# Optimization experiments

Measured on AMD Instinct MI355X. Metric: run time of the kernel, lower is better.

## Reference

```python
import jax, jax.numpy as jnp
import numpy as np

E = 128          # embedding_dim
H = 128          # decoder_hidden_dim
N = 200000       # number of candidate nodes


def setup_inputs() -> dict:
    key = jax.random.key(0)
    k0, k1, k2, k3, k4, k5 = jax.random.split(key, 6)
    return {
        "current_node_emb": jax.random.normal(k0, (1, E), jnp.float32),
        "context_emb": jax.random.normal(k1, (1, E), jnp.float32),
        "candidate_node_embs": jax.random.normal(k2, (N, E), jnp.float32),
        "Wq": jax.random.normal(k3, (H, 2 * E), jnp.float32) * 0.05,  # nn.Linear(2E->H, bias=False) weight
        "Wk": jax.random.normal(k4, (H, E), jnp.float32) * 0.05,      # nn.Linear(E->H, bias=False) weight
        "mask": jax.random.randint(k5, (1, N), 0, 2, jnp.int32),
    }


def reference(current_node_emb, context_emb, candidate_node_embs, Wq, Wk, mask):
    # combined_input = cat([current, context], dim=1) -> [1, 2E]
    combined = jnp.concatenate([current_node_emb, context_emb], axis=1)
    query = combined @ Wq.T                      # [1, H]
    keys = candidate_node_embs @ Wk.T            # [N, H]
    attn_scores = query @ keys.T                 # [1, N]
    masked = jnp.where(mask == 0, -jnp.inf, attn_scores)
    probs = jax.nn.softmax(masked, axis=1)       # [1, N]

    n = probs.shape[1]
    k = min(50, max(1, int(0.5 * n)))            # static Python int -> jit-friendly
    top_probs, _ = jax.lax.top_k(probs, k)       # [1, k]
    threshold = top_probs[:, -1:]                # [1, 1]
    top_mask = probs >= threshold
    filtered = probs * top_mask
    filtered = filtered / (jnp.sum(filtered, axis=1, keepdims=True) + 1e-10)

    log_probs_all = jnp.log(filtered + 1e-10)    # [1, N]
    # Categorical(filtered): true-zero probability outside top-k
    logits = jnp.where(filtered > 0, jnp.log(filtered), -jnp.inf)
    action_idx = jax.random.categorical(jax.random.key(42), logits, axis=1)  # [1]
    log_prob_action = jnp.take_along_axis(logits, action_idx[:, None], axis=1)[:, 0]  # [1]
    return (log_probs_all, log_prob_action, action_idx)
```

## Files before the change

### kernel.cpp

```cpp
#include <hip/hip_runtime.h>
#include <math.h>


#define CAP 4096
#define NEG_INF (-__builtin_inff())

__device__ __forceinline__ unsigned int f2ord(float f){
  unsigned int b = __float_as_uint(f);
  return (b & 0x80000000u) ? ~b : (b | 0x80000000u);
}
__device__ __forceinline__ unsigned int rotl32(unsigned int x, int d){
  return (x << d) | (x >> (32 - d));
}

__device__ float gumbel_from_idx(unsigned int idx){
  unsigned int x0 = 0u, x1 = idx;
  const unsigned int ks0 = 0u, ks1 = 42u;
  const unsigned int ks2 = 0u ^ 42u ^ 0x1BD11BDAu;
  x0 += ks0; x1 += ks1;
#define TF_RND(r) { x0 += x1; x1 = rotl32(x1, (r)); x1 ^= x0; }
  TF_RND(13) TF_RND(15) TF_RND(26) TF_RND(6)
  x0 += ks1; x1 += ks2 + 1u;
  TF_RND(17) TF_RND(29) TF_RND(16) TF_RND(24)
  x0 += ks2; x1 += ks0 + 2u;
  TF_RND(13) TF_RND(15) TF_RND(26) TF_RND(6)
  x0 += ks0; x1 += ks1 + 3u;
  TF_RND(17) TF_RND(29) TF_RND(16) TF_RND(24)
  x0 += ks1; x1 += ks2 + 4u;
  TF_RND(13) TF_RND(15) TF_RND(26) TF_RND(6)
  x0 += ks2; x1 += ks0 + 5u;
#undef TF_RND
  unsigned int bits = x0 ^ x1;
  unsigned int fb = (bits >> 9) | 0x3f800000u;
  float f = __uint_as_float(fb) - 1.0f;
  float u = (f < 1.17549435e-38f) ? 1.17549435e-38f : f;
  return -logf(-logf(u));
}

__global__ void k_prep(const float* __restrict__ cur, const float* __restrict__ ctx,
                       const float* __restrict__ Wq, const float* __restrict__ Wk,
                       float* __restrict__ v, unsigned int* __restrict__ hist,
                       unsigned int* __restrict__ scal_u){
  __shared__ float comb[256];
  __shared__ float q[128];
  int t = threadIdx.x;
  for (int k = t; k < 2048; k += 256) hist[k] = 0u;
  if (t < 8) scal_u[t] = 0u;
  comb[t] = (t < 128) ? cur[t] : ctx[t - 128];
  __syncthreads();
  if (t < 128){
    float acc = 0.f;
    const float* row = Wq + t * 256;
    for (int j = 0; j < 256; ++j) acc = fmaf(row[j], comb[j], acc);
    q[t] = acc;
  }
  __syncthreads();
  if (t < 128){
    float acc = 0.f;
    for (int h = 0; h < 128; ++h) acc = fmaf(q[h], Wk[h * 128 + t], acc);
    v[t] = acc;
  }
}

__global__ __launch_bounds__(256) void k_score(const float* __restrict__ cand,
    const int* __restrict__ mask, const float* __restrict__ v,
    float* __restrict__ scores, int N){
  int t = threadIdx.x;
  int lane = t & 63, wave = t >> 6;
  int hi = lane >> 5, hl = lane & 31;
  float4 v4 = ((const float4*)v)[hl];
  const float4* cp = (const float4*)cand;
  int base = (blockIdx.x * 4 + wave) * 16;
  float p[8];
  #pragma unroll
  for (int k = 0; k < 8; ++k){
    int r = base + 2 * k + hi;
    r = (r < N) ? r : (N - 1);
    float4 c = cp[(size_t)r * 32 + hl];
    p[k] = fmaf(c.x, v4.x, fmaf(c.y, v4.y, fmaf(c.z, v4.z, c.w * v4.w)));
  }
  #pragma unroll
  for (int k = 0; k < 8; ++k){
    p[k] += __shfl_xor(p[k], 1, 64);
    p[k] += __shfl_xor(p[k], 2, 64);
    p[k] += __shfl_xor(p[k], 4, 64);
    p[k] += __shfl_xor(p[k], 8, 64);
    p[k] += __shfl_xor(p[k], 16, 64);
  }
  float sv = p[0];
  #pragma unroll
  for (int k = 1; k < 8; ++k) sv = (hl == k) ? p[k] : sv;
  if (hl < 8){
    int r = base + 2 * hl + hi;
    if (r < N) scores[r] = mask[r] ? sv : NEG_INF;
  }
}

__global__ __launch_bounds__(256) void k_hist(const float* __restrict__ scores,
    unsigned int* __restrict__ hist, unsigned int* __restrict__ scal_u,
    int N, int ktop){
  __shared__ unsigned int lhist[2048];
  __shared__ float wsum[4];
  __shared__ int is_last;
  int t = threadIdx.x;
  int lane = t & 63, wave = t >> 6;
  for (int k = t; k < 2048; k += 256) lhist[k] = 0u;
  __syncthreads();
  float ez = 0.f;
  int i0 = (blockIdx.x * 256 + t) * 4;
  if (i0 + 3 < N){
    float4 s4 = *(const float4*)(scores + i0);
    float ss[4] = {s4.x, s4.y, s4.z, s4.w};
    #pragma unroll
    for (int e = 0; e < 4; ++e){
      if (ss[e] > NEG_INF){
        atomicAdd(&lhist[f2ord(ss[e]) >> 21], 1u);
        ez += expf(ss[e]);
      }
    }
  } else {
    for (int e = 0; e < 4; ++e){
      int i = i0 + e;
      if (i < N){
        float s = scores[i];
        if (s > NEG_INF){ atomicAdd(&lhist[f2ord(s) >> 21], 1u); ez += expf(s); }
      }
    }
  }
  #pragma unroll
  for (int off = 32; off; off >>= 1) ez += __shfl_xor(ez, off, 64);
  if (lane == 0) wsum[wave] = ez;
  __syncthreads();
  for (int k = t; k < 2048; k += 256){
    unsigned int c = lhist[k];
    if (c) atomicAdd(&hist[k], c);
  }
  if (t == 0) atomicAdd((float*)scal_u + 3, wsum[0] + wsum[1] + wsum[2] + wsum[3]);
  __syncthreads();
  if (t == 0){
    __threadfence();
    unsigned int old = atomicAdd(&scal_u[6], 1u);
    is_last = (old == gridDim.x - 1u);
  }
  __syncthreads();
  if (!is_last) return;
  __threadfence();
  __shared__ unsigned int suf[256];
  __shared__ int csel_sh;
  unsigned int csum = 0;
  for (int k = 0; k < 8; ++k) csum += hist[t * 8 + k];
  suf[t] = csum;
  if (t == 0) csel_sh = -1;
  __syncthreads();
  for (int d = 1; d < 256; d <<= 1){
    unsigned int add = (t + d < 256) ? suf[t + d] : 0u;
    __syncthreads();
    suf[t] += add;
    __syncthreads();
  }
  unsigned int st = suf[t];
  unsigned int sn = (t < 255) ? suf[t + 1] : 0u;
  if (st >= (unsigned)ktop && sn < (unsigned)ktop) csel_sh = t;
  __syncthreads();
  if (t == 0){
    int b_sel = 0;
    if (csel_sh >= 0){
      int c = csel_sh;
      unsigned int cum = (c < 255) ? suf[c + 1] : 0u;
      for (int b = 8 * c + 7; b >= 8 * c; --b){
        cum += hist[b];
        if (cum >= (unsigned)ktop){ b_sel = b; break; }
      }
    }
    scal_u[1] = ((unsigned int)b_sel) << 21;
  }
}

__global__ __launch_bounds__(256) void k_gather(const float* __restrict__ scores,
    unsigned int* __restrict__ scal_u, unsigned int* __restrict__ buf_idx,
    float* __restrict__ buf_s, float* __restrict__ out, int N, int ktop){
  int t = threadIdx.x;
  unsigned int u_lo = scal_u[1];
  int i0 = (blockIdx.x * 256 + t) * 4;
  if (i0 + 3 < N){
    float4 s4 = *(const float4*)(scores + i0);
    float ss[4] = {s4.x, s4.y, s4.z, s4.w};
    #pragma unroll
    for (int e = 0; e < 4; ++e){
      float s = ss[e];
      if (s > NEG_INF && f2ord(s) >= u_lo){
        unsigned int pos = atomicAdd(&scal_u[0], 1u);
        if (pos < CAP){ buf_idx[pos] = (unsigned int)(i0 + e); buf_s[pos] = s; }
      }
    }
  } else {
    for (int e = 0; e < 4; ++e){
      int i = i0 + e;
      if (i < N){
        float s = scores[i];
        if (s > NEG_INF && f2ord(s) >= u_lo){
          unsigned int pos = atomicAdd(&scal_u[0], 1u);
          if (pos < CAP){ buf_idx[pos] = (unsigned int)i; buf_s[pos] = s; }
        }
      }
    }
  }
  __syncthreads();
  __shared__ int is_last;
  if (t == 0){
    __threadfence();
    unsigned int old = atomicAdd(&scal_u[7], 1u);
    is_last = (old == gridDim.x - 1u);
  }
  __syncthreads();
  if (!is_last) return;
  __threadfence();
  float* scal_f = (float*)scal_u;
  __shared__ float s_lds[CAP];
  __shared__ float thr_sh;
  __shared__ float wred[4];
  __shared__ float rv[4], rl[4];
  __shared__ unsigned int ri[4];
  int C = (int)scal_u[0]; if (C > CAP) C = CAP;
  for (int j = t; j < C; j += 256) s_lds[j] = buf_s[j];
  if (t == 0) thr_sh = NEG_INF;
  __syncthreads();
  if (C > ktop){
    for (int j = t; j < C; j += 256){
      float sj = s_lds[j];
      int g = 0, e = 0;
      for (int k2 = 0; k2 < C; ++k2){
        float sk = s_lds[k2];
        g += (sk > sj);
        e += (sk == sj);
      }
      if (g < ktop && g + e >= ktop) thr_sh = sj;
    }
  }
  __syncthreads();
  float s_thr = thr_sh;
  float Z = scal_f[3];
  float part = 0.f;
  for (int j = t; j < C; j += 256){
    float sj = s_lds[j];
    if (sj >= s_thr) part += expf(sj);
  }
  #pragma unroll
  for (int off = 32; off; off >>= 1) part += __shfl_xor(part, off, 64);
  int wave = t >> 6, lane = t & 63;
  if (lane == 0) wred[wave] = part;
  __syncthreads();
  float T = wred[0] + wred[1] + wred[2] + wred[3];
  float D = T + 1e-10f * Z;
  float lnD = logf(D);
  if (t == 0){ scal_f[4] = s_thr; scal_f[5] = lnD; }
  float bestv = NEG_INF, bestlogit = NEG_INF;
  unsigned int bestidx = 0xFFFFFFFFu;
  for (int j = t; j < C; j += 256){
    float sj = s_lds[j];
    if (sj >= s_thr){
      unsigned int idx = buf_idx[j];
      float logit = sj - lnD;
      float val = logit + gumbel_from_idx(idx);
      if (val > bestv || (val == bestv && idx < bestidx)){
        bestv = val; bestlogit = logit; bestidx = idx;
      }
    }
  }
  #pragma unroll
  for (int off = 32; off; off >>= 1){
    float ov = __shfl_xor(bestv, off, 64);
    float ol = __shfl_xor(bestlogit, off, 64);
    unsigned int oi = (unsigned int)__shfl_xor((int)bestidx, off, 64);
    if (ov > bestv || (ov == bestv && oi < bestidx)){
      bestv = ov; bestlogit = ol; bestidx = oi;
    }
  }
  if (lane == 0){ rv[wave] = bestv; rl[wave] = bestlogit; ri[wave] = bestidx; }
  __syncthreads();
  if (t == 0){
    for (int w = 1; w < 4; ++w){
      if (rv[w] > rv[0] || (rv[w] == rv[0] && ri[w] < ri[0])){
        rv[0] = rv[w]; rl[0] = rl[w]; ri[0] = ri[w];
      }
    }
    out[N] = rl[0];
    out[N + 1] = (float)ri[0];
  }
}

__global__ __launch_bounds__(256) void k_final(float* __restrict__ out,
    const unsigned int* __restrict__ scal_u, int N){
  const float* scal_f = (const float*)scal_u;
  float s_thr = scal_f[4];
  float lnD = scal_f[5];
  const float NLOG = logf(1e-10f);
  int i0 = (blockIdx.x * 256 + threadIdx.x) * 4;
  if (i0 + 3 < N){
    float4 s4 = *(const float4*)(out + i0);
    float4 r;
    r.x = (s4.x >= s_thr) ? logf(expf(s4.x - lnD) + 1e-10f) : NLOG;
    r.y = (s4.y >= s_thr) ? logf(expf(s4.y - lnD) + 1e-10f) : NLOG;
    r.z = (s4.z >= s_thr) ? logf(expf(s4.z - lnD) + 1e-10f) : NLOG;
    r.w = (s4.w >= s_thr) ? logf(expf(s4.w - lnD) + 1e-10f) : NLOG;
    *(float4*)(out + i0) = r;
  } else {
    for (int e = 0; e < 4; ++e){
      int i = i0 + e;
      if (i < N){
        float s = out[i];
        out[i] = (s >= s_thr) ? logf(expf(s - lnD) + 1e-10f) : NLOG;
      }
    }
  }
}

extern "C" void kernel_launch(void* const* d_in, const int* in_sizes, int n_in,
                              void* d_out, int out_size, void* d_ws, size_t ws_size,
                              hipStream_t stream){
  const float* cur  = (const float*)d_in[0];
  const float* ctx  = (const float*)d_in[1];
  const float* cand = (const float*)d_in[2];
  const float* Wq   = (const float*)d_in[3];
  const float* Wk   = (const float*)d_in[4];
  const int*   mask = (const int*)d_in[5];
  int N = in_sizes[5];
  float* out = (float*)d_out;

  char* ws = (char*)d_ws;
  unsigned int* hist    = (unsigned int*)ws;
  float*        v       = (float*)(ws + 8192);
  unsigned int* scal_u  = (unsigned int*)(ws + 8704);
  unsigned int* buf_idx = (unsigned int*)(ws + 8768);
  float*        buf_s   = (float*)(ws + 8768 + CAP * 4);

  int ktop = N / 2; if (ktop < 1) ktop = 1; if (ktop > 50) ktop = 50;

  int g_score = (N + 63) / 64;
  int g_pass  = (N + 1023) / 1024;

  k_prep<<<1, 256, 0, stream>>>(cur, ctx, Wq, Wk, v, hist, scal_u);
  k_score<<<g_score, 256, 0, stream>>>(cand, mask, v, out, N);
  k_hist<<<g_pass, 256, 0, stream>>>(out, hist, scal_u, N, ktop);
  k_gather<<<g_pass, 256, 0, stream>>>(out, scal_u, buf_idx, buf_s, out, N, ktop);
  k_final<<<g_pass, 256, 0, stream>>>(out, scal_u, N);
}
```

Measured before the change: 208.9 us.

## Drop final pass: prefill output with log-epsilon and scatter top-k results in gather

Scores now go to a separate workspace buffer, and k_score pre-fills the output with log(1e-10). The last block of the gather kernel scatters the computed log-probs for the surviving top-k candidates directly. This removes the k_final kernel, which read and rewrote all N outputs and evaluated exp/log on each. The loads in k_score are also split from the FMAs so all eight float4 loads are issued before any arithmetic. In exchange, k_score writes an extra N floats, and the workspace layout grows to hold the scores.

```diff
diff --git a/kernel.cpp b/kernel.cpp
--- a/kernel.cpp
+++ b/kernel.cpp
@@ -45,7 +45,7 @@
   __shared__ float q[128];
   int t = threadIdx.x;
   for (int k = t; k < 2048; k += 256) hist[k] = 0u;
-  if (t < 8) scal_u[t] = 0u;
+  if (t < 16) scal_u[t] = 0u;
   comb[t] = (t < 128) ? cur[t] : ctx[t - 128];
   __syncthreads();
   if (t < 128){
@@ -64,21 +64,25 @@
 
 __global__ __launch_bounds__(256) void k_score(const float* __restrict__ cand,
     const int* __restrict__ mask, const float* __restrict__ v,
-    float* __restrict__ scores, int N){
+    float* __restrict__ scores, float* __restrict__ out, int N){
+  const float NLOG = logf(1e-10f);
   int t = threadIdx.x;
   int lane = t & 63, wave = t >> 6;
   int hi = lane >> 5, hl = lane & 31;
   float4 v4 = ((const float4*)v)[hl];
   const float4* cp = (const float4*)cand;
   int base = (blockIdx.x * 4 + wave) * 16;
-  float p[8];
+  float4 c[8];
   #pragma unroll
   for (int k = 0; k < 8; ++k){
     int r = base + 2 * k + hi;
     r = (r < N) ? r : (N - 1);
-    float4 c = cp[(size_t)r * 32 + hl];
-    p[k] = fmaf(c.x, v4.x, fmaf(c.y, v4.y, fmaf(c.z, v4.z, c.w * v4.w)));
-  }
+    c[k] = cp[(size_t)r * 32 + hl];
+  }
+  float p[8];
+  #pragma unroll
+  for (int k = 0; k < 8; ++k)
+    p[k] = fmaf(c[k].x, v4.x, fmaf(c[k].y, v4.y, fmaf(c[k].z, v4.z, c[k].w * v4.w)));
   #pragma unroll
   for (int k = 0; k < 8; ++k){
     p[k] += __shfl_xor(p[k], 1, 64);
@@ -94,6 +98,8 @@
     int r = base + 2 * hl + hi;
     if (r < N) scores[r] = mask[r] ? sv : NEG_INF;
   }
+  int rr = blockIdx.x * 64 + t;
+  if (t < 64 && rr < N) out[rr] = NLOG;
 }
 
 __global__ __launch_bounds__(256) void k_hist(const float* __restrict__ scores,
@@ -253,7 +259,10 @@
   float T = wred[0] + wred[1] + wred[2] + wred[3];
   float D = T + 1e-10f * Z;
   float lnD = logf(D);
-  if (t == 0){ scal_f[4] = s_thr; scal_f[5] = lnD; }
+  for (int j = t; j < C; j += 256){
+    float sj = s_lds[j];
+    if (sj >= s_thr) out[buf_idx[j]] = logf(expf(sj - lnD) + 1e-10f);
+  }
   float bestv = NEG_INF, bestlogit = NEG_INF;
   unsigned int bestidx = 0xFFFFFFFFu;
   for (int j = t; j < C; j += 256){
@@ -286,32 +295,6 @@
     }
     out[N] = rl[0];
     out[N + 1] = (float)ri[0];
-  }
-}
-
-__global__ __launch_bounds__(256) void k_final(float* __restrict__ out,
-    const unsigned int* __restrict__ scal_u, int N){
-  const float* scal_f = (const float*)scal_u;
-  float s_thr = scal_f[4];
-  float lnD = scal_f[5];
-  const float NLOG = logf(1e-10f);
-  int i0 = (blockIdx.x * 256 + threadIdx.x) * 4;
-  if (i0 + 3 < N){
-    float4 s4 = *(const float4*)(out + i0);
-    float4 r;
-    r.x = (s4.x >= s_thr) ? logf(expf(s4.x - lnD) + 1e-10f) : NLOG;
-    r.y = (s4.y >= s_thr) ? logf(expf(s4.y - lnD) + 1e-10f) : NLOG;
-    r.z = (s4.z >= s_thr) ? logf(expf(s4.z - lnD) + 1e-10f) : NLOG;
-    r.w = (s4.w >= s_thr) ? logf(expf(s4.w - lnD) + 1e-10f) : NLOG;
-    *(float4*)(out + i0) = r;
-  } else {
-    for (int e = 0; e < 4; ++e){
-      int i = i0 + e;
-      if (i < N){
-        float s = out[i];
-        out[i] = (s >= s_thr) ? logf(expf(s - lnD) + 1e-10f) : NLOG;
-      }
-    }
   }
 }
 
@@ -328,11 +311,13 @@
   float* out = (float*)d_out;
 
   char* ws = (char*)d_ws;
-  unsigned int* hist    = (unsigned int*)ws;
-  float*        v       = (float*)(ws + 8192);
-  unsigned int* scal_u  = (unsigned int*)(ws + 8704);
-  unsigned int* buf_idx = (unsigned int*)(ws + 8768);
-  float*        buf_s   = (float*)(ws + 8768 + CAP * 4);
+  unsigned int* scal_u  = (unsigned int*)ws;
+  unsigned int* hist    = (unsigned int*)(ws + 256);
+  float*        v       = (float*)(ws + 256 + 8192);
+  float*        scores  = (float*)(ws + 256 + 8192 + 512);
+  char*         bufbase = ws + 256 + 8192 + 512 + 800000;
+  unsigned int* buf_idx = (unsigned int*)bufbase;
+  float*        buf_s   = (float*)(bufbase + CAP * 4);
 
   int ktop = N / 2; if (ktop < 1) ktop = 1; if (ktop > 50) ktop = 50;
 
@@ -340,8 +325,7 @@
   int g_pass  = (N + 1023) / 1024;
 
   k_prep<<<1, 256, 0, stream>>>(cur, ctx, Wq, Wk, v, hist, scal_u);
-  k_score<<<g_score, 256, 0, stream>>>(cand, mask, v, out, N);
-  k_hist<<<g_pass, 256, 0, stream>>>(out, hist, scal_u, N, ktop);
-  k_gather<<<g_pass, 256, 0, stream>>>(out, scal_u, buf_idx, buf_s, out, N, ktop);
-  k_final<<<g_pass, 256, 0, stream>>>(out, scal_u, N);
-}
+  k_score<<<g_score, 256, 0, stream>>>(cand, mask, v, scores, out, N);
+  k_hist<<<g_pass, 256, 0, stream>>>(scores, hist, scal_u, N, ktop);
+  k_gather<<<g_pass, 256, 0, stream>>>(scores, scal_u, buf_idx, buf_s, out, N, ktop);
+}
```

Result: no change. 206.5 us (-1.1%).
